# Optimization experiments

Measured on AMD Instinct MI355X. Metric: run time of the kernel, lower is better.

The kernel has to match this reference:

```python
import jax, jax.numpy as jnp
import numpy as np

# config[4]: SparseConv3d(32, 64, k=3, stride=2, pad=1) on a (21,800,704) voxel grid, nnz=220939
IN_DIMS = (21, 800, 704)   # (x, y, z) spatial extents
KSIZE   = (3, 3, 3)
STRIDE  = (2, 2, 2)
PAD     = (1, 1, 1)
CIN, COUT = 32, 64
NNZ = 220939
OUT_DIMS = tuple((IN_DIMS[d] + 2 * PAD[d] - KSIZE[d]) // STRIDE[d] + 1 for d in range(3))  # (11,400,352)


def setup_inputs() -> dict:
    key = jax.random.key(0)
    k1, k2, k3 = jax.random.split(key, 3)
    features = jax.random.normal(k1, (NNZ, CIN), dtype=jnp.float32)
    coords = jnp.stack(
        [jax.random.randint(jax.random.fold_in(k2, d), (NNZ,), 0, IN_DIMS[d]) for d in range(3)],
        axis=1,
    ).astype(jnp.int32)
    # spconv weight layout: one [Cin, Cout] GEMM per kernel offset (27 offsets)
    weight = jax.random.normal(k3, (KSIZE[0] * KSIZE[1] * KSIZE[2], CIN, COUT), dtype=jnp.float32) * 0.05
    return {"features": features, "coords": coords, "weight": weight}


def reference(features, coords, weight):
    # Rulebook gather-GEMM-scatter, vectorized over points; static loop over 27 offsets.
    # out[o] += W[k] @ in[i] where i = o*stride - pad + k, i.e. o = (coord_i + pad - k)/stride.
    n_out = OUT_DIMS[0] * OUT_DIMS[1] * OUT_DIMS[2]
    stride = jnp.array(STRIDE, jnp.int32)
    pad = jnp.array(PAD, jnp.int32)
    odims = jnp.array(OUT_DIMS, jnp.int32)
    out = jnp.zeros((n_out + 1, COUT), features.dtype)  # last row = dump slot for invalid
    kidx = 0
    for kx in range(KSIZE[0]):
        for ky in range(KSIZE[1]):
            for kz in range(KSIZE[2]):
                off = jnp.array([kx, ky, kz], jnp.int32)
                o = coords + pad - off                      # [N,3]
                oq = o // stride
                valid = jnp.all((o >= 0) & (o % stride == 0) & (oq < odims), axis=1)
                flat = (oq[:, 0] * OUT_DIMS[1] + oq[:, 1]) * OUT_DIMS[2] + oq[:, 2]
                flat = jnp.where(valid, flat, n_out)
                contrib = features @ weight[kidx]           # [N, Cout] per-offset GEMM
                out = out.at[flat].add(contrib)             # scatter-accumulate
                kidx += 1
    # Densified sparse-conv output (inactive output sites are exactly zero)
    return out[:-1].reshape(OUT_DIMS + (COUT,))
```

## Files before the change

kernel.cpp:

```cpp
#include <hip/hip_runtime.h>


#define CIN  32
#define COUT 64
#define OXD  11
#define OYD  400
#define OZD  352
#define NSITES (OXD * OYD * OZD)

constexpr int CHUNKS = 96;

__global__ __launch_bounds__(256) void zero_out_k(float4* __restrict__ out4,
                                                  int n4, int* __restrict__ gcnt) {
    const int i = blockIdx.x * 256 + threadIdx.x;
    if (i < n4) out4[i] = make_float4(0.f, 0.f, 0.f, 0.f);
    if (i < 27) gcnt[i] = 0;
}

__global__ __launch_bounds__(256) void build_pairs(
    const int* __restrict__ coords, int2* __restrict__ arena,
    int* __restrict__ gcnt, int nnz)
{
    __shared__ int lcnt[27];
    __shared__ int lbase[27];
    const int t = threadIdx.x;
    if (t < 27) lcnt[t] = 0;
    __syncthreads();

    const int n = blockIdx.x * 256 + t;
    int ncomb = 0;
    int ck[8], cls[8], csite[8];
    if (n < nnz) {
        const int cx = coords[3 * n + 0];
        const int cy = coords[3 * n + 1];
        const int cz = coords[3 * n + 2];
        int kxl[2], oxl[2], nx;
        int kyl[2], oyl[2], ny;
        int kzl[2], ozl[2], nz;
        {
            const int c1 = cx + 1;
            if (c1 & 1) { kxl[0] = 1; oxl[0] = c1 >> 1; nx = 1; }
            else { kxl[0] = 2; oxl[0] = (c1 - 2) >> 1; nx = 1;
                   if ((c1 >> 1) < OXD) { kxl[1] = 0; oxl[1] = c1 >> 1; nx = 2; } }
        }
        {
            const int c1 = cy + 1;
            if (c1 & 1) { kyl[0] = 1; oyl[0] = c1 >> 1; ny = 1; }
            else { kyl[0] = 2; oyl[0] = (c1 - 2) >> 1; ny = 1;
                   if ((c1 >> 1) < OYD) { kyl[1] = 0; oyl[1] = c1 >> 1; ny = 2; } }
        }
        {
            const int c1 = cz + 1;
            if (c1 & 1) { kzl[0] = 1; ozl[0] = c1 >> 1; nz = 1; }
            else { kzl[0] = 2; ozl[0] = (c1 - 2) >> 1; nz = 1;
                   if ((c1 >> 1) < OZD) { kzl[1] = 0; ozl[1] = c1 >> 1; nz = 2; } }
        }
        for (int ix = 0; ix < nx; ++ix)
            for (int iy = 0; iy < ny; ++iy)
                for (int iz = 0; iz < nz; ++iz) {
                    const int k = kxl[ix] * 9 + kyl[iy] * 3 + kzl[iz];
                    const int site = (oxl[ix] * OYD + oyl[iy]) * OZD + ozl[iz];
                    ck[ncomb] = k;
                    csite[ncomb] = site;
                    cls[ncomb] = atomicAdd(&lcnt[k], 1);
                    ++ncomb;
                }
    }
    __syncthreads();
    if (t < 27) lbase[t] = atomicAdd(&gcnt[t], lcnt[t]);
    __syncthreads();
    for (int c = 0; c < ncomb; ++c) {
        const int k = ck[c];
        arena[(size_t)k * nnz + lbase[k] + cls[c]] = make_int2(n, csite[c]);
    }
}

__global__ __launch_bounds__(256) void spconv_scatter(
    const float* __restrict__ feat,
    const float* __restrict__ weight,
    const int2*  __restrict__ arena,
    const int*   __restrict__ gcnt,
    float*       __restrict__ out,
    int nnz)
{
    const int lane = threadIdx.x & 63;
    const int k     = blockIdx.x % 27;
    const int chunk = blockIdx.x / 27;
    const int cnt = gcnt[k];
    if (cnt == 0) return;

    float w[CIN];
    const float* __restrict__ Wk = weight + (size_t)k * CIN * COUT;
    #pragma unroll
    for (int ci = 0; ci < CIN; ++ci) w[ci] = Wk[ci * COUT + lane];

    const int NW = CHUNKS * 4;
    const int widk = chunk * 4 + (threadIdx.x >> 6);
    const int C = (cnt + NW - 1) / NW;
    const int start = widk * C;
    const int end   = min(start + C, cnt);
    const int2* __restrict__ ak = arena + (size_t)k * nnz;

    for (int i0 = start; i0 < end; i0 += 64) {
        const int take = min(64, end - i0);
        int idx = i0 + lane;
        if (idx >= end) idx = end - 1;
        const int2 pr = ak[idx];

        for (int j = 0; j < take; ++j) {
            const int pt = __builtin_amdgcn_readlane(pr.x, j);
            const int st = __builtin_amdgcn_readlane(pr.y, j);
            const float* __restrict__ fr = feat + (size_t)pt * CIN;
            float a0 = 0.f, a1 = 0.f, a2 = 0.f, a3 = 0.f;
            #pragma unroll
            for (int ci = 0; ci < CIN; ci += 4) {
                a0 = fmaf(fr[ci + 0], w[ci + 0], a0);
                a1 = fmaf(fr[ci + 1], w[ci + 1], a1);
                a2 = fmaf(fr[ci + 2], w[ci + 2], a2);
                a3 = fmaf(fr[ci + 3], w[ci + 3], a3);
            }
            atomicAdd(out + (size_t)st * COUT + lane, (a0 + a1) + (a2 + a3));
        }
    }
}

extern "C" void kernel_launch(void* const* d_in, const int* in_sizes, int n_in,
                              void* d_out, int out_size, void* d_ws, size_t ws_size,
                              hipStream_t stream) {
    const float* feat   = (const float*)d_in[0];
    const int*   coords = (const int*)d_in[1];
    const float* weight = (const float*)d_in[2];
    float*       out    = (float*)d_out;
    const int nnz = in_sizes[0] / CIN;

    int2* arena = (int2*)d_ws;
    int*  gcnt  = (int*)(arena + (size_t)27 * nnz);

    const int n4 = out_size / 4;
    zero_out_k<<<(n4 + 255) / 256, 256, 0, stream>>>((float4*)out, n4, gcnt);
    build_pairs<<<(nnz + 255) / 256, 256, 0, stream>>>(coords, arena, gcnt, nnz);
    spconv_scatter<<<27 * CHUNKS, 256, 0, stream>>>(feat, weight, arena, gcnt, out, nnz);
}
```

Baseline: 583.6 us.

## Stage gathered feature rows in LDS and use packed FMA in scatter kernel

Each lane now loads one full feature row with coalesced float4 loads into a per-wave LDS tile, and the inner loop reads rows from LDS by broadcast. Before, every lane fetched the same scalar feature values from global memory. The dot product also uses 2-wide vector FMA so the compiler can emit packed FP32 instructions. This adds LDS use of 32KB per block, which may limit occupancy. The gather is now done once per 64-pair batch rather than per pair.

```diff
diff --git a/kernel.cpp b/kernel.cpp
--- a/kernel.cpp
+++ b/kernel.cpp
@@ -6,9 +6,10 @@
 #define OXD  11
 #define OYD  400
 #define OZD  352
-#define NSITES (OXD * OYD * OZD)
 
 constexpr int CHUNKS = 96;
+
+typedef float v2f __attribute__((ext_vector_type(2)));
 
 __global__ __launch_bounds__(256) void zero_out_k(float4* __restrict__ out4,
                                                   int n4, int* __restrict__ gcnt) {
@@ -83,43 +84,64 @@
     float*       __restrict__ out,
     int nnz)
 {
+    __shared__ float lds[4][8][64][4];
+
     const int lane = threadIdx.x & 63;
+    const int wid  = threadIdx.x >> 6;
     const int k     = blockIdx.x % 27;
     const int chunk = blockIdx.x / 27;
     const int cnt = gcnt[k];
     if (cnt == 0) return;
 
-    float w[CIN];
+    v2f w2[16];
     const float* __restrict__ Wk = weight + (size_t)k * CIN * COUT;
     #pragma unroll
-    for (int ci = 0; ci < CIN; ++ci) w[ci] = Wk[ci * COUT + lane];
+    for (int i = 0; i < 16; ++i) {
+        w2[i][0] = Wk[(2 * i + 0) * COUT + lane];
+        w2[i][1] = Wk[(2 * i + 1) * COUT + lane];
+    }
 
     const int NW = CHUNKS * 4;
-    const int widk = chunk * 4 + (threadIdx.x >> 6);
+    const int widk = chunk * 4 + wid;
     const int C = (cnt + NW - 1) / NW;
     const int start = widk * C;
     const int end   = min(start + C, cnt);
     const int2* __restrict__ ak = arena + (size_t)k * nnz;
+    float* __restrict__ outl = out + lane;
 
     for (int i0 = start; i0 < end; i0 += 64) {
         const int take = min(64, end - i0);
-        int idx = i0 + lane;
-        if (idx >= end) idx = end - 1;
+        const int idx = min(i0 + lane, end - 1);
         const int2 pr = ak[idx];
 
+        const float4* __restrict__ fr4 = (const float4*)(feat + (size_t)pr.x * CIN);
+        float4 r[8];
+        #pragma unroll
+        for (int b = 0; b < 8; ++b) r[b] = fr4[b];
+        #pragma unroll
+        for (int b = 0; b < 8; ++b) *(float4*)&lds[wid][b][lane][0] = r[b];
+        asm volatile("s_waitcnt lgkmcnt(0)" ::: "memory");
+
         for (int j = 0; j < take; ++j) {
-            const int pt = __builtin_amdgcn_readlane(pr.x, j);
+            v2f a0 = {0.f, 0.f}, a1 = {0.f, 0.f};
+            #pragma unroll
+            for (int b = 0; b < 8; ++b) {
+                const float4 f = *(const float4*)&lds[wid][b][j][0];
+                v2f f01 = {f.x, f.y};
+                v2f f23 = {f.z, f.w};
+#if __has_builtin(__builtin_elementwise_fma)
+                a0 = __builtin_elementwise_fma(f01, w2[2 * b + 0], a0);
+                a1 = __builtin_elementwise_fma(f23, w2[2 * b + 1], a1);
+#else
+                a0[0] = fmaf(f01[0], w2[2 * b + 0][0], a0[0]);
+                a0[1] = fmaf(f01[1], w2[2 * b + 0][1], a0[1]);
+                a1[0] = fmaf(f23[0], w2[2 * b + 1][0], a1[0]);
+                a1[1] = fmaf(f23[1], w2[2 * b + 1][1], a1[1]);
+#endif
+            }
             const int st = __builtin_amdgcn_readlane(pr.y, j);
-            const float* __restrict__ fr = feat + (size_t)pt * CIN;
-            float a0 = 0.f, a1 = 0.f, a2 = 0.f, a3 = 0.f;
-            #pragma unroll
-            for (int ci = 0; ci < CIN; ci += 4) {
-                a0 = fmaf(fr[ci + 0], w[ci + 0], a0);
-                a1 = fmaf(fr[ci + 1], w[ci + 1], a1);
-                a2 = fmaf(fr[ci + 2], w[ci + 2], a2);
-                a3 = fmaf(fr[ci + 3], w[ci + 3], a3);
-            }
-            atomicAdd(out + (size_t)st * COUT + lane, (a0 + a1) + (a2 + a3));
+            const float acc = (a0[0] + a0[1]) + (a1[0] + a1[1]);
+            atomicAdd(outl + (size_t)st * COUT, acc);
         }
     }
 }
```

Result: faster. 570.9 us (-2.2%).
